# Kernel tuning notes

Measured on AMD Instinct MI355X. Metric: run time of the kernel, lower is better.

## Reference

```python
import jax, jax.numpy as jnp
import numpy as np

B, S, D, E = 2, 2048, 1024, 8
H = 2 * D          # hidden_dim = 2*n_embd
A = H // 16        # adapt_dim


def _ln(x, g, b):
    m = x.mean(-1, keepdims=True)
    v = x.var(-1, keepdims=True)
    return (x - m) * jax.lax.rsqrt(v + 1e-5) * g + b


def setup_inputs() -> dict:
    key = jax.random.key(0)
    ks = jax.random.split(key, 16)
    s = 1.0 / np.sqrt(D)        # shared-linear init scale
    sa = s * 0.01               # adapter-linear init scale
    sg = 0.01 / np.sqrt(A)      # expert adapter init scale
    f32 = jnp.float32
    return {
        "x": jax.random.normal(ks[0], (B, S, D), f32),
        "expert_weights": jax.nn.softmax(jax.random.normal(ks[1], (B * S, E), f32), -1),
        "up_w": jax.random.normal(ks[2], (H, D), f32) * s,
        "gate_w": jax.random.normal(ks[3], (H, D), f32) * s,
        "down_w": jax.random.normal(ks[4], (D, H), f32) * s,
        "pre_w": jax.random.normal(ks[5], (A, D), f32) * sa,
        "post_w": jax.random.normal(ks[6], (A, H), f32) * sa,
        "an_g": jnp.ones((A,), f32),
        "an_b": jnp.zeros((A,), f32),
        "adapt_proj_w": jax.random.normal(ks[7], (H, A), f32) * sa,
        "adapter_w": jax.random.normal(ks[8], (E, A, A), f32) * sg,
        "adapter_g": jnp.ones((E, A), f32),
        "adapter_b": jnp.zeros((E, A), f32),
        "expert_proj_w": jax.random.normal(ks[9], (H, A), f32) * sg,
        "output_proj_w": jax.random.normal(ks[10], (D, H), f32) * sg,
    }


def reference(x, expert_weights, up_w, gate_w, down_w, pre_w, post_w, an_g, an_b,
              adapt_proj_w, adapter_w, adapter_g, adapter_b, expert_proj_w, output_proj_w):
    # ---- SharedExpertMLP ----
    up = x @ up_w.T                                  # [B,S,H]
    gate = x @ gate_w.T                              # [B,S,H]
    hidden = jax.nn.silu(gate) * up                  # SwiGLU
    adapt_in = _ln(x @ pre_w.T, an_g, an_b)          # [B,S,A]
    adapt_out = _ln(hidden @ post_w.T, an_g, an_b)   # [B,S,A]
    w = jnp.einsum('bsa,bta->bst', adapt_in, adapt_out)
    w = jax.nn.silu(jnp.clip(w, -5.0, 5.0))          # clamp+SiLU score
    # explicit fp32 bmm as in original autocast-disabled block
    adapt = jnp.einsum('bst,bta->bsa',
                       w.astype(jnp.float32),
                       adapt_in.astype(jnp.float32)).astype(x.dtype)
    hidden = hidden + 0.1 * (adapt @ adapt_proj_w.T)
    shared_out = hidden @ down_w.T                   # [B,S,D] (dropout is identity in eval)

    # ---- per-token expert mixing ----
    xf = x.reshape(-1, x.shape[-1])                  # [N,D], N=B*S
    a = _ln(xf @ pre_w.T, an_g, an_b)                # [N,A]
    h = jnp.einsum('na,eca->nec', a, adapter_w)      # per-expert low-rank adapt [N,E,A]
    h = _ln(h, adapter_g[None], adapter_b[None])
    mixed = jnp.einsum('ne,nea->na', expert_weights, h)   # combine experts [N,A]
    out = (mixed @ expert_proj_w.T) @ output_proj_w.T     # [N,D]
    return shared_out + out.reshape(x.shape)
```

## Files before the change

### kernel.cpp

```cpp
#include <hip/hip_runtime.h>
#include <hip/hip_bf16.h>
#include <math.h>

#define Bq 2
#define Sq 2048
#define Dq 1024
#define Eq 8
#define Hq 2048
#define Aq 128
#define Nq (Bq*Sq)

typedef __attribute__((ext_vector_type(4))) float f32x4;
typedef __attribute__((ext_vector_type(8))) short bfrag;

__device__ __forceinline__ float silu_f(float x) {
    return x / (1.0f + expf(-x));
}
__device__ __forceinline__ unsigned short f2bf(float x) {
    unsigned u = __float_as_uint(x);
    u += 0x7fffu + ((u >> 16) & 1u);
    return (unsigned short)(u >> 16);
}
__device__ __forceinline__ float bf2f(unsigned short h) {
    return __uint_as_float(((unsigned)h) << 16);
}
__device__ __forceinline__ void gl16(const unsigned short* g, unsigned short* l) {
    __builtin_amdgcn_global_load_lds(
        (const __attribute__((address_space(1))) void*)g,
        (__attribute__((address_space(3))) void*)(void*)l, 16, 0, 0);
}

#define WAITV_BAR(N)                                            \
    asm volatile("s_waitcnt vmcnt(" #N ")" ::: "memory");       \
    __builtin_amdgcn_s_barrier();                               \
    asm volatile("" ::: "memory")
#define END_BAR()                                               \
    asm volatile("" ::: "memory");                              \
    __builtin_amdgcn_s_barrier();                               \
    asm volatile("" ::: "memory")

__global__ __launch_bounds__(256)
void convert_all(const float* __restrict__ x,  const float* __restrict__ gw,
                 const float* __restrict__ uw, const float* __restrict__ dw,
                 const float* __restrict__ pw, const float* __restrict__ ow,
                 const float* __restrict__ opw, const float* __restrict__ aw,
                 unsigned short* xh,  unsigned short* gwh, unsigned short* uwh,
                 unsigned short* dwh, unsigned short* pwh, unsigned short* powh,
                 unsigned short* oph, unsigned short* adw)
{
    const int T = 3276800;
    for (int i = blockIdx.x * 256 + threadIdx.x; i < T; i += gridDim.x * 256) {
        const float* in; unsigned short* hi; int j = i;
        if (j < 1048576)                 { in = x;   hi = xh;  }
        else if ((j -= 1048576) < 524288){ in = gw;  hi = gwh; }
        else if ((j -= 524288) < 524288) { in = uw;  hi = uwh; }
        else if ((j -= 524288) < 524288) { in = dw;  hi = dwh; }
        else if ((j -= 524288) < 32768)  { in = pw;  hi = pwh; }
        else if ((j -= 32768) < 65536)   { in = ow;  hi = powh; }
        else if ((j -= 65536) < 524288)  { in = opw; hi = oph; }
        else { j -= 524288;                in = aw;  hi = adw; }
        float4 v = ((const float4*)in)[j];
        ((ushort4*)hi)[j] = make_ushort4(f2bf(v.x), f2bf(v.y), f2bf(v.z), f2bf(v.w));
    }
}

template<typename TIN>
__global__ __launch_bounds__(256)
void transb(const TIN* __restrict__ in, unsigned short* __restrict__ out, int R, int C)
{
    __shared__ float t[32][33];
    in  += (size_t)blockIdx.z * R * C;
    out += (size_t)blockIdx.z * R * C;
    int tx = threadIdx.x & 31, ty = threadIdx.x >> 5;
    int r0 = blockIdx.y * 32, c0 = blockIdx.x * 32;
#pragma unroll
    for (int j = 0; j < 4; j++) {
        TIN v = in[(size_t)(r0 + ty + j * 8) * C + c0 + tx];
        float f;
        if (sizeof(TIN) == 2) f = bf2f(*(const unsigned short*)&v);
        else                  f = *(const float*)&v;
        t[ty + j * 8][tx] = f;
    }
    __syncthreads();
#pragma unroll
    for (int j = 0; j < 4; j++)
        out[(size_t)(c0 + ty + j * 8) * R + r0 + tx] = f2bf(t[tx][ty + j * 8]);
}

template<int EPI>
__global__ __launch_bounds__(512)
void mg(const unsigned short* __restrict__ Ah, const unsigned short* __restrict__ Bh,
        void* __restrict__ Cv, int N, int K, int kchunks,
        long zA, long zB, long zC, long pz)
{
    __shared__ __align__(16) unsigned short lds[32768];

    const int tid = threadIdx.x;
    const int l   = tid & 63;
    const int w   = tid >> 6;
    const int wr  = w >> 2, wc = w & 3;
    const int bm0 = blockIdx.y * 128, bn0 = blockIdx.x * 128;
    const int bz  = blockIdx.z / kchunks;
    const int kz  = blockIdx.z - bz * kchunks;
    const int kcnt = K / kchunks;
    const int kbeg = kz * kcnt;
    const int kend = kbeg + kcnt;

    const unsigned short* A0 = Ah + (size_t)bz * zA;
    const unsigned short* B0 = Bh + (size_t)bz * zB;

    const int srow = tid >> 3;
    const int sq   = (tid & 7) ^ (srow & 7);
    const size_t aoff = (size_t)(bm0 + srow) * K + sq * 8;
    const size_t boff = (size_t)(bn0 + srow) * K + sq * 8;
    const size_t r64  = (size_t)64 * K;

    auto stage = [&](int b, int kt) {
        unsigned short* d = &lds[b * 16384 + (w << 9)];
        gl16(A0 + aoff + kt,       d + 0);
        gl16(A0 + aoff + kt + r64, d + 4096);
        gl16(B0 + boff + kt,       d + 8192);
        gl16(B0 + boff + kt + r64, d + 12288);
    };

    const int rowa = (wr * 64 + (l & 15)) * 64;
    const int rowb = (wc * 32 + (l & 15)) * 64;
    const int q0 = (((l >> 4)    ) ^ (l & 7)) << 3;
    const int q1 = (((l >> 4) + 4) ^ (l & 7)) << 3;

    f32x4 acc[4][2];
#pragma unroll
    for (int i = 0; i < 4; i++)
#pragma unroll
        for (int j = 0; j < 2; j++) acc[i][j] = (f32x4){0.f, 0.f, 0.f, 0.f};

    stage(0, kbeg);
    int cur = 0;
    for (int kt = kbeg; kt < kend; kt += 64) {
        if (kt + 64 < kend) {
            stage(cur ^ 1, kt + 64);
            WAITV_BAR(4);
        } else {
            WAITV_BAR(0);
        }
        const int cb = cur * 16384;
#pragma unroll
        for (int ks = 0; ks < 2; ks++) {
            const int qo = ks ? q1 : q0;
            bfrag a4[4], b4[2];
#pragma unroll
            for (int f = 0; f < 4; f++)
                a4[f] = *(const bfrag*)&lds[cb + rowa + f * 1024 + qo];
#pragma unroll
            for (int f = 0; f < 2; f++)
                b4[f] = *(const bfrag*)&lds[cb + 8192 + rowb + f * 1024 + qo];
#pragma unroll
            for (int i = 0; i < 4; i++)
#pragma unroll
                for (int j = 0; j < 2; j++)
                    acc[i][j] = __builtin_amdgcn_mfma_f32_16x16x32_bf16(a4[i], b4[j], acc[i][j], 0, 0, 0);
        }
        END_BAR();
        cur ^= 1;
    }

    const int crow0 = bm0 + wr * 64 + (l >> 4) * 4;
    const int ccol0 = bn0 + wc * 32 + (l & 15);
#pragma unroll
    for (int i = 0; i < 4; i++)
#pragma unroll
        for (int j = 0; j < 2; j++)
#pragma unroll
            for (int r = 0; r < 4; r++) {
                size_t idx = (size_t)(crow0 + i * 16 + r) * N + (ccol0 + j * 16);
                float v = acc[i][j][r];
                if (EPI == 0)
                    ((float*)Cv + (size_t)bz * zC + (size_t)kz * pz)[idx] = v;
                else
                    ((unsigned short*)Cv + (size_t)bz * zC)[idx] =
                        f2bf(silu_f(fminf(fmaxf(v, -5.f), 5.f)));
            }
}

__global__ __launch_bounds__(512)
void gup(const unsigned short* __restrict__ xh, const unsigned short* __restrict__ gwh,
         const unsigned short* __restrict__ uwh, unsigned short* __restrict__ hh)
{
    __shared__ __align__(16) unsigned short lds[24576];
    const int tid = threadIdx.x;
    const int l   = tid & 63;
    const int w   = tid >> 6;
    const int wr  = w >> 2, wc = w & 3;

    int id  = blockIdx.y * gridDim.x + blockIdx.x;
    int xcd = id & 7, j = id >> 3;
    int bx  = (xcd & 1) * 8 + (j & 7);
    int by  = (xcd >> 1) * 8 + (j >> 3);
    const int bm0 = by * 128, bn0 = bx * 128;

    const int srow = tid >> 2;
    const int sq   = (tid & 3) ^ ((srow >> 1) & 3);
    const size_t aoff = (size_t)(bm0 + srow) * Dq + sq * 8;
    const size_t boff = (size_t)(bn0 + srow) * Dq + sq * 8;

    const int rowa = (wr * 64 + (l & 15)) * 32;
    const int rowb = (wc * 32 + (l & 15)) * 32;
    const int q0 = (((l >> 4)) ^ (((l & 15) >> 1) & 3)) << 3;

    auto stage = [&](int b, int kt) {
        unsigned short* d = &lds[b * 12288 + (w << 9)];
        gl16(xh  + aoff + kt, d + 0);
        gl16(gwh + boff + kt, d + 4096);
        gl16(uwh + boff + kt, d + 8192);
    };

    f32x4 accg[4][2], accu[4][2];
#pragma unroll
    for (int i = 0; i < 4; i++)
#pragma unroll
        for (int jj = 0; jj < 2; jj++) {
            accg[i][jj] = (f32x4){0.f, 0.f, 0.f, 0.f};
            accu[i][jj] = (f32x4){0.f, 0.f, 0.f, 0.f};
        }

    stage(0, 0);
    int cur = 0;
    for (int kt = 0; kt < Dq; kt += 32) {
        if (kt + 32 < Dq) {
            stage(cur ^ 1, kt + 32);
            WAITV_BAR(3);
        } else {
            WAITV_BAR(0);
        }
        const int cb = cur * 12288;
        bfrag a4[4], g4[2], u4[2];
#pragma unroll
        for (int f = 0; f < 4; f++)
            a4[f] = *(const bfrag*)&lds[cb + rowa + f * 512 + q0];
#pragma unroll
        for (int f = 0; f < 2; f++) {
            g4[f] = *(const bfrag*)&lds[cb + 4096 + rowb + f * 512 + q0];
            u4[f] = *(const bfrag*)&lds[cb + 8192 + rowb + f * 512 + q0];
        }
#pragma unroll
        for (int i = 0; i < 4; i++)
#pragma unroll
            for (int jj = 0; jj < 2; jj++) {
                accg[i][jj] = __builtin_amdgcn_mfma_f32_16x16x32_bf16(a4[i], g4[jj], accg[i][jj], 0, 0, 0);
                accu[i][jj] = __builtin_amdgcn_mfma_f32_16x16x32_bf16(a4[i], u4[jj], accu[i][jj], 0, 0, 0);
            }
        END_BAR();
        cur ^= 1;
    }

    const int crow0 = bm0 + wr * 64 + (l >> 4) * 4;
    const int ccol0 = bn0 + wc * 32 + (l & 15);
#pragma unroll
    for (int i = 0; i < 4; i++)
#pragma unroll
        for (int jj = 0; jj < 2; jj++)
#pragma unroll
            for (int r = 0; r < 4; r++) {
                size_t idx = (size_t)(crow0 + i * 16 + r) * Hq + (ccol0 + jj * 16);
                hh[idx] = f2bf(silu_f(accg[i][jj][r]) * accu[i][jj][r]);
            }
}

__global__ __launch_bounds__(512)
void gfinal(const unsigned short* __restrict__ hh, const unsigned short* __restrict__ dwh,
            const unsigned short* __restrict__ acat, const unsigned short* __restrict__ kcat,
            float* __restrict__ out)
{
    __shared__ __align__(16) unsigned short lds[49152];
    const int tid = threadIdx.x;
    const int l   = tid & 63;
    const int w   = tid >> 6;
    const int wr  = w >> 2, wc = w & 3;

    int nb  = gridDim.x * gridDim.y;
    int id  = blockIdx.y * gridDim.x + blockIdx.x;
    int id2 = (id & 7) * (nb >> 3) + (id >> 3);
    int bx  = id2 % gridDim.x, by = id2 / gridDim.x;
    const int bm0 = by * 128, bn0 = bx * 128;

    const int srow = tid >> 3;
    const int sq   = (tid & 7) ^ (srow & 7);
    const int rowa = (wr * 64 + (l & 15)) * 64;
    const int rowb = (wc * 32 + (l & 15)) * 64;
    const int q0 = (((l >> 4)    ) ^ (l & 7)) << 3;
    const int q1 = (((l >> 4) + 4) ^ (l & 7)) << 3;

    f32x4 acc[4][2];
#pragma unroll
    for (int i = 0; i < 4; i++)
#pragma unroll
        for (int j = 0; j < 2; j++) acc[i][j] = (f32x4){0.f, 0.f, 0.f, 0.f};

    {
        const size_t aoff = (size_t)(bm0 + srow) * Hq + sq * 8;
        const size_t boff = (size_t)(bn0 + srow) * Hq + sq * 8;
        const size_t r64  = (size_t)64 * Hq;
        auto stage = [&](int b, int kt) {
            unsigned short* d = &lds[b * 16384 + (w << 9)];
            gl16(hh  + aoff + kt,       d + 0);
            gl16(hh  + aoff + kt + r64, d + 4096);
            gl16(dwh + boff + kt,       d + 8192);
            gl16(dwh + boff + kt + r64, d + 12288);
        };
        stage(0, 0);
        stage(1, 64);
        int cur = 0;
        for (int kt = 0; kt < Hq; kt += 64) {
            if (kt + 64 < Hq) { WAITV_BAR(4); } else { WAITV_BAR(0); }
            if (kt + 128 < Hq) {
                int nb3 = (cur + 2 >= 3) ? cur - 1 : cur + 2;
                stage(nb3, kt + 128);
            }
            const int cb = cur * 16384;
#pragma unroll
            for (int ks = 0; ks < 2; ks++) {
                const int qo = ks ? q1 : q0;
                bfrag a4[4], b4[2];
#pragma unroll
                for (int f = 0; f < 4; f++)
                    a4[f] = *(const bfrag*)&lds[cb + rowa + f * 1024 + qo];
#pragma unroll
                for (int f = 0; f < 2; f++)
                    b4[f] = *(const bfrag*)&lds[cb + 8192 + rowb + f * 1024 + qo];
#pragma unroll
                for (int i = 0; i < 4; i++)
#pragma unroll
                    for (int j = 0; j < 2; j++)
                        acc[i][j] = __builtin_amdgcn_mfma_f32_16x16x32_bf16(a4[i], b4[j], acc[i][j], 0, 0, 0);
            }
            cur = (cur == 2) ? 0 : cur + 1;
        }
    }
    END_BAR();
    {
        const size_t aoff = (size_t)(bm0 + srow) * 256 + sq * 8;
        const size_t boff = (size_t)(bn0 + srow) * 256 + sq * 8;
        const size_t r64  = (size_t)64 * 256;
        auto stage2 = [&](int b, int kt) {
            unsigned short* d = &lds[b * 16384 + (w << 9)];
            gl16(acat + aoff + kt,       d + 0);
            gl16(acat + aoff + kt + r64, d + 4096);
            gl16(kcat + boff + kt,       d + 8192);
            gl16(kcat + boff + kt + r64, d + 12288);
        };
        stage2(0, 0);
        stage2(1, 64);
        int cur = 0;
        for (int kt = 0; kt < 256; kt += 64) {
            if (kt + 64 < 256) { WAITV_BAR(4); } else { WAITV_BAR(0); }
            if (kt + 128 < 256) {
                int nb3 = (cur + 2 >= 3) ? cur - 1 : cur + 2;
                stage2(nb3, kt + 128);
            }
            const int cb = cur * 16384;
#pragma unroll
            for (int ks = 0; ks < 2; ks++) {
                const int qo = ks ? q1 : q0;
                bfrag a4[4], b4[2];
#pragma unroll
                for (int f = 0; f < 4; f++)
                    a4[f] = *(const bfrag*)&lds[cb + rowa + f * 1024 + qo];
#pragma unroll
                for (int f = 0; f < 2; f++)
                    b4[f] = *(const bfrag*)&lds[cb + 8192 + rowb + f * 1024 + qo];
#pragma unroll
                for (int i = 0; i < 4; i++)
#pragma unroll
                    for (int j = 0; j < 2; j++)
                        acc[i][j] = __builtin_amdgcn_mfma_f32_16x16x32_bf16(a4[i], b4[j], acc[i][j], 0, 0, 0);
            }
            cur = (cur == 2) ? 0 : cur + 1;
        }
    }

    const int crow0 = bm0 + wr * 64 + (l >> 4) * 4;
    const int ccol0 = bn0 + wc * 32 + (l & 15);
#pragma unroll
    for (int i = 0; i < 4; i++)
#pragma unroll
        for (int j = 0; j < 2; j++)
#pragma unroll
            for (int r = 0; r < 4; r++)
                out[(size_t)(crow0 + i * 16 + r) * Dq + ccol0 + j * 16] = acc[i][j][r];
}

template<int NZ>
__global__ __launch_bounds__(256)
void rln(const float* __restrict__ p, unsigned short* __restrict__ oh,
         const float* __restrict__ g, const float* __restrict__ b, long pstride)
{
    int row  = blockIdx.x * 4 + (threadIdx.x >> 6);
    int lane = threadIdx.x & 63;
    long base = (long)row * Aq;
    float x0 = 0.f, x1 = 0.f;
#pragma unroll
    for (int z = 0; z < NZ; z++) {
        x0 += p[base + z * pstride + lane];
        x1 += p[base + z * pstride + lane + 64];
    }
    float s  = x0 + x1;
    float ss = x0 * x0 + x1 * x1;
#pragma unroll
    for (int off = 32; off > 0; off >>= 1) {
        s  += __shfl_xor(s, off);
        ss += __shfl_xor(ss, off);
    }
    float m  = s * (1.0f / Aq);
    float v  = ss * (1.0f / Aq) - m * m;
    float rs = rsqrtf(v + 1e-5f);
    oh[base + lane]      = f2bf((x0 - m) * rs * g[lane]      + b[lane]);
    oh[base + lane + 64] = f2bf((x1 - m) * rs * g[lane + 64] + b[lane + 64]);
}

template<int NZ>
__global__ __launch_bounds__(256)
void rbf(const float* __restrict__ p, unsigned short* __restrict__ o,
         int rowsPerB, float scale, int total, int ostride, int ocol, int ocolStep)
{
    int i = blockIdx.x * 256 + threadIdx.x;
    if (i >= total) return;
    int n = i >> 7, a = i & 127;
    int bz = n / rowsPerB, s = n - bz * rowsPerB;
    long base = ((long)bz * NZ) * rowsPerB * Aq + (long)s * Aq + a;
    float acc = 0.f;
#pragma unroll
    for (int z = 0; z < NZ; z++) acc += p[base + (long)z * rowsPerB * Aq];
    o[(long)s * ostride + (ocol + bz * ocolStep) + a +
      (ocolStep ? 0 : (long)bz * rowsPerB * ostride)] = f2bf(acc * scale);
}

__global__ __launch_bounds__(256)
void mix_ln(const float* __restrict__ h, const float* __restrict__ ew,
            const float* __restrict__ g, const float* __restrict__ bb,
            unsigned short* __restrict__ acat)
{
    int n    = blockIdx.x * 4 + (threadIdx.x >> 6);
    int lane = threadIdx.x & 63;
    float a0 = 0.0f, a1 = 0.0f;
#pragma unroll
    for (int e = 0; e < Eq; e++) {
        const float* r = h + ((long)e * Nq + n) * Aq;
        float x0 = r[lane], x1 = r[lane + 64];
        float s  = x0 + x1;
        float ss = x0 * x0 + x1 * x1;
#pragma unroll
        for (int off = 32; off > 0; off >>= 1) {
            s  += __shfl_xor(s, off);
            ss += __shfl_xor(ss, off);
        }
        float m  = s * (1.0f / Aq);
        float v  = ss * (1.0f / Aq) - m * m;
        float rs = rsqrtf(v + 1e-5f);
        float wv = ew[(long)n * Eq + e];
        a0 += wv * ((x0 - m) * rs * g[e * Aq + lane]      + bb[e * Aq + lane]);
        a1 += wv * ((x1 - m) * rs * g[e * Aq + lane + 64] + bb[e * Aq + lane + 64]);
    }
    acat[(long)n * 256 + 128 + lane]      = f2bf(a0);
    acat[(long)n * 256 + 128 + lane + 64] = f2bf(a1);
}

extern "C" void kernel_launch(void* const* d_in, const int* in_sizes, int n_in,
                              void* d_out, int out_size, void* d_ws, size_t ws_size,
                              hipStream_t stream)
{
    const float* x             = (const float*)d_in[0];
    const float* ew            = (const float*)d_in[1];
    const float* up_w          = (const float*)d_in[2];
    const float* gate_w        = (const float*)d_in[3];
    const float* down_w        = (const float*)d_in[4];
    const float* pre_w         = (const float*)d_in[5];
    const float* post_w        = (const float*)d_in[6];
    const float* an_g          = (const float*)d_in[7];
    const float* an_b          = (const float*)d_in[8];
    const float* adapt_proj_w  = (const float*)d_in[9];
    const float* adapter_w     = (const float*)d_in[10];
    const float* adapter_g     = (const float*)d_in[11];
    const float* adapter_b     = (const float*)d_in[12];
    const float* expert_proj_w = (const float*)d_in[13];
    const float* output_proj_w = (const float*)d_in[14];
    float* out = (float*)d_out;

#define OFF(kb) ((char*)d_ws + (size_t)(kb) * 1024)
    float* kdp  = (float*)OFF(0);
    float* wfp  = (float*)OFF(8192);
    float* p1   = (float*)OFF(16384);
    float* p2   = (float*)OFF(0);
    unsigned short* wmat = (unsigned short*)OFF(16384);
    float* p3   = (float*)OFF(0);
    float* h_e  = (float*)OFF(0);
    unsigned short* hh   = (unsigned short*)OFF(32768);
    unsigned short* xh   = (unsigned short*)OFF(49152);
    unsigned short* gwh  = (unsigned short*)OFF(57344);
    unsigned short* uwh  = (unsigned short*)OFF(61440);
    unsigned short* dwh  = (unsigned short*)OFF(65536);
    unsigned short* oph  = (unsigned short*)OFF(69632);
    unsigned short* pwh  = (unsigned short*)OFF(73728);
    unsigned short* powh = (unsigned short*)OFF(73984);
    unsigned short* apT  = (unsigned short*)OFF(74496);
    unsigned short* epT  = (unsigned short*)OFF(75008);
    unsigned short* ainh = (unsigned short*)OFF(75520);
    unsigned short* ainT = (unsigned short*)OFF(76544);
    unsigned short* aouth= (unsigned short*)OFF(77568);
    unsigned short* adw  = (unsigned short*)OFF(78592);
    unsigned short* kcat = (unsigned short*)OFF(78848);
    unsigned short* acat = (unsigned short*)OFF(79360);
#undef OFF

    dim3 blk(256), blk512(512);
    const long NA = (long)Nq * Aq;
    const long SA = (long)Sq * Aq;
    const long SS = (long)Sq * Sq;

    convert_all<<<dim3(2048), blk, 0, stream>>>(x, gate_w, up_w, down_w, pre_w, post_w,
        output_proj_w, adapter_w, xh, gwh, uwh, dwh, pwh, powh, oph, adw);
    transb<float><<<dim3(4, 64, 1), blk, 0, stream>>>(adapt_proj_w,  apT, Hq, Aq);
    transb<float><<<dim3(4, 64, 1), blk, 0, stream>>>(expert_proj_w, epT, Hq, Aq);

    mg<0><<<dim3(1, 8, 32), blk512, 0, stream>>>(dwh, apT, kdp, Aq, Hq, 16,
        (long)Dq * Hq, (long)Aq * Hq, (long)16 * Dq * Aq, (long)Dq * Aq);
    rbf<16><<<dim3(1024), blk, 0, stream>>>(kdp, kcat, Dq, 1.0f, 2 * Dq * Aq, 256, 0, 128);

    mg<0><<<dim3(1, 32, 8), blk512, 0, stream>>>(xh, pwh, p1, Aq, Dq, 8, 0, 0, 0, NA);
    rln<8><<<dim3(1024), blk, 0, stream>>>(p1, ainh, an_g, an_b, NA);
    transb<unsigned short><<<dim3(4, 64, 2), blk, 0, stream>>>(ainh, ainT, Sq, Aq);

    gup<<<dim3(16, 32), blk512, 0, stream>>>(xh, gwh, uwh, hh);

    mg<0><<<dim3(1, 32, 8), blk512, 0, stream>>>(hh, powh, p2, Aq, Hq, 8, 0, 0, 0, NA);
    rln<8><<<dim3(1024), blk, 0, stream>>>(p2, aouth, an_g, an_b, NA);

    mg<1><<<dim3(16, 16, 2), blk512, 0, stream>>>(ainh, aouth, wmat, Sq, Aq, 1,
        SA, SA, SS, 0);

    mg<0><<<dim3(1, 16, 16), blk512, 0, stream>>>(wmat, ainT, p3, Aq, Sq, 8,
        SS, SA, 8 * SA, SA);
    rbf<8><<<dim3(2048), blk, 0, stream>>>(p3, acat, Sq, 0.1f, Nq * Aq, 256, 0, 0);

    mg<0><<<dim3(1, 32, 8), blk512, 0, stream>>>(ainh, adw, h_e, Aq, Aq, 1,
        0, (long)Aq * Aq, NA, 0);
    mix_ln<<<dim3(1024), blk, 0, stream>>>(h_e, ew, adapter_g, adapter_b, acat);

    gfinal<<<dim3(8, 32), blk512, 0, stream>>>(hh, dwh, acat, kcat, out);
}
```

Before: 165.0 us.

## Fuse score GEMM and score-weighted GEMM into one flash-style kernel

Replaces the two launches that wrote the 2048x2048 bf16 clamp-SiLU score matrix to global memory and then multiplied it by adapt_in transposed. A single kernel now computes each 128x128 score tile in LDS, applies clamp+SiLU, and immediately multiplies it by the matching adapt_in^T tile, accumulating partial results per split. This removes the score matrix round-trip through HBM and one launch, at the cost of 128KB of LDS per block and lower occupancy. The two weight-transpose launches are also merged into one launch using the z grid dimension, relying on epT sitting directly after apT in the workspace.

```diff
diff --git a/kernel.cpp b/kernel.cpp
--- a/kernel.cpp
+++ b/kernel.cpp
@@ -66,10 +66,12 @@
 
 template<typename TIN>
 __global__ __launch_bounds__(256)
-void transb(const TIN* __restrict__ in, unsigned short* __restrict__ out, int R, int C)
+void transb(const TIN* __restrict__ in0, const TIN* __restrict__ in1,
+            unsigned short* __restrict__ out, int R, int C)
 {
     __shared__ float t[32][33];
-    in  += (size_t)blockIdx.z * R * C;
+    const TIN* in = blockIdx.z ? in1 : in0;
+    if (!in1) in = in0 + (size_t)blockIdx.z * R * C;
     out += (size_t)blockIdx.z * R * C;
     int tx = threadIdx.x & 31, ty = threadIdx.x >> 5;
     int r0 = blockIdx.y * 32, c0 = blockIdx.x * 32;
@@ -180,6 +182,126 @@
                     ((unsigned short*)Cv + (size_t)bz * zC)[idx] =
                         f2bf(silu_f(fminf(fmaxf(v, -5.f), 5.f)));
             }
+}
+
+__global__ __launch_bounds__(512)
+void gsc(const unsigned short* __restrict__ ainh, const unsigned short* __restrict__ aouth,
+         const unsigned short* __restrict__ ainT, float* __restrict__ p3)
+{
+    __shared__ __align__(16) unsigned short lds[65536];
+    const int AIN = 0, AOUT = 16384, AINT = 32768, PB = 49152;
+
+    const int tid = threadIdx.x;
+    const int l   = tid & 63;
+    const int w   = tid >> 6;
+    const int wr  = w >> 2, wc = w & 3;
+    const int tz  = blockIdx.x;
+    const int ib  = blockIdx.y;
+    const int b   = blockIdx.z;
+    const long SA = (long)Sq * Aq;
+
+    auto stage32 = [&](int base, const unsigned short* src, size_t kstride) {
+#pragma unroll
+        for (int rd = 0; rd < 4; rd++) {
+            int grow = rd * 32 + (w << 2) + (l >> 4);
+            int slot = (l & 15) ^ (grow & 15);
+            gl16(src + (size_t)grow * kstride + slot * 8,
+                 &lds[base + rd * 4096 + (w << 9)]);
+        }
+    };
+
+    const unsigned short* ainI_src = ainh + (size_t)b * SA + (size_t)(ib * 128) * Aq;
+    f32x4 acc2[4][2];
+#pragma unroll
+    for (int i = 0; i < 4; i++)
+#pragma unroll
+        for (int j = 0; j < 2; j++) acc2[i][j] = (f32x4){0.f, 0.f, 0.f, 0.f};
+
+    {
+        int tglob = tz * 2;
+        stage32(AIN,  ainI_src, Aq);
+        stage32(AOUT, aouth + (size_t)b * SA + (size_t)(tglob * 128) * Aq, Aq);
+        stage32(AINT, ainT  + (size_t)b * SA + (size_t)(tglob * 128), Sq);
+        WAITV_BAR(0);
+    }
+
+    const int rowa = (wr * 64 + (l & 15)) * 128;
+    const int rowb = (wc * 32 + (l & 15)) * 128;
+
+#pragma unroll 1
+    for (int t = 0; t < 2; t++) {
+        if (t == 1) {
+            int tglob = tz * 2 + 1;
+            stage32(AOUT, aouth + (size_t)b * SA + (size_t)(tglob * 128) * Aq, Aq);
+            stage32(AINT, ainT  + (size_t)b * SA + (size_t)(tglob * 128), Sq);
+            WAITV_BAR(0);
+        }
+        f32x4 acc1[4][2];
+#pragma unroll
+        for (int i = 0; i < 4; i++)
+#pragma unroll
+            for (int j = 0; j < 2; j++) acc1[i][j] = (f32x4){0.f, 0.f, 0.f, 0.f};
+#pragma unroll
+        for (int ks = 0; ks < 4; ks++) {
+            const int qo = ((ks * 4 + (l >> 4)) ^ (l & 15)) << 3;
+            bfrag a4[4], b4[2];
+#pragma unroll
+            for (int f = 0; f < 4; f++)
+                a4[f] = *(const bfrag*)&lds[AIN + rowa + f * 2048 + qo];
+#pragma unroll
+            for (int f = 0; f < 2; f++)
+                b4[f] = *(const bfrag*)&lds[AOUT + rowb + f * 2048 + qo];
+#pragma unroll
+            for (int i = 0; i < 4; i++)
+#pragma unroll
+                for (int j = 0; j < 2; j++)
+                    acc1[i][j] = __builtin_amdgcn_mfma_f32_16x16x32_bf16(a4[i], b4[j], acc1[i][j], 0, 0, 0);
+        }
+        {
+            const int prow0 = wr * 64 + (l >> 4) * 4;
+            const int pcol0 = wc * 32 + (l & 15);
+#pragma unroll
+            for (int i = 0; i < 4; i++)
+#pragma unroll
+                for (int j = 0; j < 2; j++)
+#pragma unroll
+                    for (int r = 0; r < 4; r++) {
+                        int pr = prow0 + i * 16 + r;
+                        int pc = pcol0 + j * 16;
+                        float v = silu_f(fminf(fmaxf(acc1[i][j][r], -5.f), 5.f));
+                        lds[PB + pr * 128 + (((pc >> 3) ^ (pr & 15)) << 3) + (pc & 7)] = f2bf(v);
+                    }
+        }
+        __syncthreads();
+#pragma unroll
+        for (int ks = 0; ks < 4; ks++) {
+            const int qo = ((ks * 4 + (l >> 4)) ^ (l & 15)) << 3;
+            bfrag a4[4], b4[2];
+#pragma unroll
+            for (int f = 0; f < 4; f++)
+                a4[f] = *(const bfrag*)&lds[PB + rowa + f * 2048 + qo];
+#pragma unroll
+            for (int f = 0; f < 2; f++)
+                b4[f] = *(const bfrag*)&lds[AINT + rowb + f * 2048 + qo];
+#pragma unroll
+            for (int i = 0; i < 4; i++)
+#pragma unroll
+                for (int j = 0; j < 2; j++)
+                    acc2[i][j] = __builtin_amdgcn_mfma_f32_16x16x32_bf16(a4[i], b4[j], acc2[i][j], 0, 0, 0);
+        }
+        __syncthreads();
+    }
+
+    const int crow0 = wr * 64 + (l >> 4) * 4;
+    const int ccol0 = wc * 32 + (l & 15);
+    float* dst = p3 + ((size_t)(b * 8 + tz) * Sq + ib * 128) * Aq;
+#pragma unroll
+    for (int i = 0; i < 4; i++)
+#pragma unroll
+        for (int j = 0; j < 2; j++)
+#pragma unroll
+            for (int r = 0; r < 4; r++)
+                dst[(size_t)(crow0 + i * 16 + r) * Aq + ccol0 + j * 16] = acc2[i][j][r];
 }
 
 __global__ __launch_bounds__(512)
@@ -490,7 +612,6 @@
     float* wfp  = (float*)OFF(8192);
     float* p1   = (float*)OFF(16384);
     float* p2   = (float*)OFF(0);
-    unsigned short* wmat = (unsigned short*)OFF(16384);
     float* p3   = (float*)OFF(0);
     float* h_e  = (float*)OFF(0);
     unsigned short* hh   = (unsigned short*)OFF(32768);
@@ -518,8 +639,8 @@
 
     convert_all<<<dim3(2048), blk, 0, stream>>>(x, gate_w, up_w, down_w, pre_w, post_w,
         output_proj_w, adapter_w, xh, gwh, uwh, dwh, pwh, powh, oph, adw);
-    transb<float><<<dim3(4, 64, 1), blk, 0, stream>>>(adapt_proj_w,  apT, Hq, Aq);
-    transb<float><<<dim3(4, 64, 1), blk, 0, stream>>>(expert_proj_w, epT, Hq, Aq);
+    transb<float><<<dim3(4, 64, 2), blk, 0, stream>>>(adapt_proj_w, expert_proj_w,
+        apT, Hq, Aq);
 
     mg<0><<<dim3(1, 8, 32), blk512, 0, stream>>>(dwh, apT, kdp, Aq, Hq, 16,
         (long)Dq * Hq, (long)Aq * Hq, (long)16 * Dq * Aq, (long)Dq * Aq);
@@ -527,18 +648,15 @@
 
     mg<0><<<dim3(1, 32, 8), blk512, 0, stream>>>(xh, pwh, p1, Aq, Dq, 8, 0, 0, 0, NA);
     rln<8><<<dim3(1024), blk, 0, stream>>>(p1, ainh, an_g, an_b, NA);
-    transb<unsigned short><<<dim3(4, 64, 2), blk, 0, stream>>>(ainh, ainT, Sq, Aq);
+    transb<unsigned short><<<dim3(4, 64, 2), blk, 0, stream>>>(ainh, nullptr,
+        ainT, Sq, Aq);
 
     gup<<<dim3(16, 32), blk512, 0, stream>>>(xh, gwh, uwh, hh);
 
     mg<0><<<dim3(1, 32, 8), blk512, 0, stream>>>(hh, powh, p2, Aq, Hq, 8, 0, 0, 0, NA);
     rln<8><<<dim3(1024), blk, 0, stream>>>(p2, aouth, an_g, an_b, NA);
 
-    mg<1><<<dim3(16, 16, 2), blk512, 0, stream>>>(ainh, aouth, wmat, Sq, Aq, 1,
-        SA, SA, SS, 0);
-
-    mg<0><<<dim3(1, 16, 16), blk512, 0, stream>>>(wmat, ainT, p3, Aq, Sq, 8,
-        SS, SA, 8 * SA, SA);
+    gsc<<<dim3(8, 16, 2), blk512, 0, stream>>>(ainh, aouth, ainT, p3);
     rbf<8><<<dim3(2048), blk, 0, stream>>>(p3, acat, Sq, 0.1f, Nq * Aq, 256, 0, 0);
 
     mg<0><<<dim3(1, 32, 8), blk512, 0, stream>>>(ainh, adw, h_e, Aq, Aq, 1,
```

Result: no change. 164.6 us (-0.3%).
